# Kernel tuning notes

Measured on AMD Instinct MI355X. Metric: run time of the kernel, lower is better.

## Reference

```python
import jax, jax.numpy as jnp
import numpy as np

G, IN_DIM, OUT_DIM = 100000, 256, 128
B, N = 4096, 8192
ALPHA = 0.2          # LeakyReLU negative slope
NEG_INF = -9e15      # same masking constant as the torch module
EPS = 1e-12          # F.normalize eps


def setup_inputs() -> dict:
    key = jax.random.key(0)
    k1, k2, k3, k4, k5, k6, k7 = jax.random.split(key, 7)
    global_feature = jax.random.normal(k1, (G, IN_DIM), dtype=jnp.float32)
    nodes = jax.random.randint(k2, (B,), 0, G, dtype=jnp.int32)
    unique_nodes = jax.random.randint(k3, (N,), 0, G, dtype=jnp.int32)
    mask = jax.random.randint(k4, (B, N), 0, 2, dtype=jnp.int32)
    # ensure every row has at least one neighbor (original always includes self)
    mask = mask.at[:, 0].set(1)
    # xavier_uniform with gain=1.414
    gain = 1.414
    lim_W = gain * np.sqrt(6.0 / (IN_DIM + OUT_DIM))
    W = jax.random.uniform(k5, (IN_DIM, OUT_DIM), jnp.float32, -lim_W, lim_W)
    lim_a = gain * np.sqrt(6.0 / (2 * OUT_DIM + 1))
    a1 = jax.random.uniform(k6, (OUT_DIM,), jnp.float32, -lim_a, lim_a)
    a2 = jax.random.uniform(k7, (OUT_DIM,), jnp.float32, -lim_a, lim_a)
    return {"global_feature": global_feature, "nodes": nodes,
            "unique_nodes": unique_nodes, "mask": mask,
            "W": W, "a1": a1, "a2": a2}


def reference(global_feature, nodes, unique_nodes, mask, W, a1, a2):
    # project gathered features: [B,F], [N,F]
    h_nodes = global_feature[nodes] @ W
    h_neigh = global_feature[unique_nodes] @ W
    # additive attention scores; equivalent to cat([h_i,h_j]) @ a
    e = h_nodes @ a1[:, None] + (h_neigh @ a2)[None, :]   # [B,N]
    e = jnp.where(e >= 0, e, ALPHA * e)                    # leaky relu
    e = jnp.where(mask > 0, e, NEG_INF)
    attention = jax.nn.softmax(e, axis=1)                  # [B,N]
    out = attention @ h_neigh                              # [B,F]
    norm = jnp.linalg.norm(out, axis=1, keepdims=True)
    out = out / jnp.maximum(norm, EPS)                     # F.normalize p=2
    return out
```

## Files before the change

### kernel.cpp

```cpp
#include <hip/hip_runtime.h>
#include <hip/hip_bf16.h>

#define IN_DIM  256
#define OUT_DIM 128
#define B_ROWS  4096
#define N_COLS  8192
#define ALPHA   0.2f
#define NS      16

typedef unsigned short u16;
typedef unsigned int   u32;
typedef __attribute__((ext_vector_type(8))) short short8;
typedef __attribute__((ext_vector_type(4))) float floatx4;

__device__ __forceinline__ float bf2f(u16 v){ return __uint_as_float(((u32)v) << 16); }
__device__ __forceinline__ float bflo(u32 v){ return __uint_as_float(v << 16); }
__device__ __forceinline__ float bfhi(u32 v){ return __uint_as_float(v & 0xffff0000u); }
__device__ __forceinline__ u16 f2bf(float f){
    u32 u = __float_as_uint(f);
    u += 0x7fffu + ((u >> 16) & 1u);
    return (u16)(u >> 16);
}
__device__ __forceinline__ u32 pack_bf16(float a, float b){
    __hip_bfloat162 h = __float22bfloat162_rn(make_float2(a, b));
    return *reinterpret_cast<u32*>(&h);
}

__device__ __forceinline__ int detect_bf16_wave(const u32* __restrict__ g){
    int lane = threadIdx.x & 63;
    uint4 u = ((const uint4*)g)[lane];
#define CHK(x) ((((x) >> 7) & 0xFF) >= 110 && (((x) >> 7) & 0xFF) <= 140)
    unsigned long long c0 = __ballot(CHK(u.x)), c1 = __ballot(CHK(u.y));
    unsigned long long c2 = __ballot(CHK(u.z)), c3 = __ballot(CHK(u.w));
#undef CHK
    int votes = __popcll(c0) + __popcll(c1) + __popcll(c2) + __popcll(c3);
    return votes >= 128;
}

__global__ __launch_bounds__(128) void k_prep(const void* __restrict__ gf,
                                              const void* __restrict__ W, const void* __restrict__ a1,
                                              const void* __restrict__ a2,
                                              u16* __restrict__ WB, float* __restrict__ Wa1,
                                              float* __restrict__ a2f){
    const int isbf = detect_bf16_wave((const u32*)gf);
    const int c  = threadIdx.x;
    const int kb = blockIdx.x;
    float a1c = isbf ? bf2f(((const u16*)a1)[c]) : ((const float*)a1)[c];
    float w[8]; short8 v;
#pragma unroll
    for (int j = 0; j < 8; j++){
        w[j] = isbf ? bf2f(((const u16*)W)[(kb*8 + j) * OUT_DIM + c])
                    : ((const float*)W)[(kb*8 + j) * OUT_DIM + c];
        v[j] = (short)f2bf(w[j]);
    }
    ((short8*)WB)[kb * OUT_DIM + c] = v;

    __shared__ float red[2][8];
    int lane = c & 63, wv = c >> 6;
#pragma unroll
    for (int j = 0; j < 8; j++){
        float p = w[j] * a1c;
        p += __shfl_xor(p, 1);  p += __shfl_xor(p, 2);  p += __shfl_xor(p, 4);
        p += __shfl_xor(p, 8);  p += __shfl_xor(p, 16); p += __shfl_xor(p, 32);
        if (lane == 0) red[wv][j] = p;
    }
    __syncthreads();
    if (c < 8) Wa1[kb*8 + c] = red[0][c] + red[1][c];
    if (kb == 0) a2f[c] = isbf ? bf2f(((const u16*)a2)[c]) : ((const float*)a2)[c];
}

#define HN_BLKS 512
#define ESN_BLKS 1024
#define ZERO_BLKS 128
__global__ __launch_bounds__(256) void k_mid(const void* __restrict__ gf, const int* __restrict__ uniq,
                                             const int* __restrict__ nodes,
                                             const u16* __restrict__ WB, const float* __restrict__ a2f,
                                             const float* __restrict__ Wa1,
                                             u16* __restrict__ hB, float2* __restrict__ esg2,
                                             float2* __restrict__ esn2, float* __restrict__ oacc){
    const int bid = blockIdx.x;
    const int t   = threadIdx.x;

    if (bid < HN_BLKS){
        const int n0   = bid * 16;
        const int lane = t & 63;
        const int wv   = t >> 6;
        const int q    = lane >> 4;
        const int m    = lane & 15;
        const int isbf = detect_bf16_wave((const u32*)gf);
        const int jb0  = wv * 2;

        const size_t row = (size_t)uniq[n0 + m];
        const short8* wb8 = (const short8*)WB;

        floatx4 acc0 = {0.f,0.f,0.f,0.f};
        floatx4 acc1 = {0.f,0.f,0.f,0.f};

#pragma unroll
        for (int ks = 0; ks < IN_DIM/32; ks++){
            short8 afrag;
            if (isbf){
                afrag = *(const short8*)((const u16*)gf + row * IN_DIM + ks*32 + q*8);
            } else {
                const float* gp = (const float*)gf + row * IN_DIM + ks*32 + q*8;
                float4 f0 = *(const float4*)gp;
                float4 f1 = *(const float4*)(gp + 4);
                afrag[0] = (short)f2bf(f0.x); afrag[1] = (short)f2bf(f0.y);
                afrag[2] = (short)f2bf(f0.z); afrag[3] = (short)f2bf(f0.w);
                afrag[4] = (short)f2bf(f1.x); afrag[5] = (short)f2bf(f1.y);
                afrag[6] = (short)f2bf(f1.z); afrag[7] = (short)f2bf(f1.w);
            }
            const int kb = ks*4 + q;
            short8 b0 = wb8[kb * OUT_DIM + jb0*16 + m];
            short8 b1 = wb8[kb * OUT_DIM + (jb0+1)*16 + m];
            acc0 = __builtin_amdgcn_mfma_f32_16x16x32_bf16(afrag, b0, acc0, 0, 0, 0);
            acc1 = __builtin_amdgcn_mfma_f32_16x16x32_bf16(afrag, b1, acc1, 0, 0, 0);
        }

        {
            uint2 v0, v1;
            v0.x = pack_bf16(acc0[0], acc0[1]);
            v0.y = pack_bf16(acc0[2], acc0[3]);
            v1.x = pack_bf16(acc1[0], acc1[1]);
            v1.y = pack_bf16(acc1[2], acc1[3]);
            u16* base = hB + (size_t)(n0/8 + (q>>1)) * 1024 + (q&1)*4;
            *(uint2*)(base + (jb0*16 + m) * 8)     = v0;
            *(uint2*)(base + ((jb0+1)*16 + m) * 8) = v1;
        }

        __shared__ float sred[4][16];
        float a2c0 = a2f[jb0*16 + m], a2c1 = a2f[(jb0+1)*16 + m];
#pragma unroll
        for (int reg = 0; reg < 4; reg++){
            float pr = acc0[reg]*a2c0 + acc1[reg]*a2c1;
            pr += __shfl_xor(pr, 1); pr += __shfl_xor(pr, 2);
            pr += __shfl_xor(pr, 4); pr += __shfl_xor(pr, 8);
            if (m == 0) sred[wv][q*4 + reg] = pr;
        }
        __syncthreads();
        if (t < 16){
            float s = sred[0][t] + sred[1][t] + sred[2][t] + sred[3][t];
            s = fminf(fmaxf(s, -40.f), 40.f);
            esg2[n0 + t] = make_float2(__expf(s), __expf(ALPHA * s));
        }
    } else if (bid < HN_BLKS + ESN_BLKS){
        const int eb = bid - HN_BLKS;
        int lane = t & 63, wv = t >> 6;
        int b = eb * 4 + wv;
        const int isbf = detect_bf16_wave((const u32*)gf);
        float4 wa = ((const float4*)Wa1)[lane];
        float x0, x1, x2, x3;
        if (isbf){
            uint2 gg = ((const uint2*)((const u16*)gf + (size_t)nodes[b] * IN_DIM))[lane];
            x0 = bflo(gg.x); x1 = bfhi(gg.x); x2 = bflo(gg.y); x3 = bfhi(gg.y);
        } else {
            float4 gg = ((const float4*)((const float*)gf + (size_t)nodes[b] * IN_DIM))[lane];
            x0 = gg.x; x1 = gg.y; x2 = gg.z; x3 = gg.w;
        }
        float s = x0*wa.x + x1*wa.y + x2*wa.z + x3*wa.w;
        s += __shfl_xor(s, 1);  s += __shfl_xor(s, 2);  s += __shfl_xor(s, 4);
        s += __shfl_xor(s, 8);  s += __shfl_xor(s, 16); s += __shfl_xor(s, 32);
        if (lane == 0){
            s = fminf(fmaxf(s, -40.f), 40.f);
            esn2[b] = make_float2(__expf(s), __expf(ALPHA * s));
        }
    } else {
        const int zb = bid - (HN_BLKS + ESN_BLKS);
        float4* dst = (float4*)(oacc + (size_t)zb * (B_ROWS*OUT_DIM/ZERO_BLKS));
        float4 z = {0.f,0.f,0.f,0.f};
#pragma unroll
        for (int i = 0; i < 4; i++)
            dst[t + i*256] = z;
    }
}

template<int USE_PART>
__global__ __launch_bounds__(128, 4) void k_attn(const int* __restrict__ mask,
                                                 const float2* __restrict__ esn2,
                                                 const float2* __restrict__ esg2,
                                                 const u16* __restrict__ hB,
                                                 float* __restrict__ obuf){
    const int bid = blockIdx.x;
    const int ns  = bid & (NS-1);
    const int rg  = bid >> 4;
    const int t = threadIdx.x, lane = t & 63, wv = t >> 6;
    const int q = lane >> 4, m = lane & 15;
    const int rowbase = rg*32 + wv*16;
    const int row = rowbase + m;
    const int n0  = ns * (N_COLS/NS);

    __shared__ float4 seg[256];
    {
        const float4* egsrc = (const float4*)esg2 + (n0 >> 1);
        seg[t]       = egsrc[t];
        seg[t + 128] = egsrc[t + 128];
    }
    __syncthreads();

    const float2 en = esn2[row];
    const float enx = en.x, eny = en.y;
    const int* mrow = mask + (size_t)row * N_COLS;
    const short8* hb8 = (const short8*)hB;

    floatx4 acc[8];
#pragma unroll
    for (int jb = 0; jb < 8; jb++){ floatx4 z = {0.f,0.f,0.f,0.f}; acc[jb] = z; }

#pragma unroll 4
    for (int ks = 0; ks < 16; ks++){
        const int nn = n0 + ks*32;
        int4 ma = *(const int4*)(mrow + nn + q*8);
        int4 mb = *(const int4*)(mrow + nn + q*8 + 4);
        const float4* egl = &seg[ks*16 + q*4];
        float4 g0 = egl[0], g1 = egl[1], g2 = egl[2], g3 = egl[3];

        float p[8];
#define PEL(j, mk, gx, gy) { float tt = fmaxf(enx * (gx), eny * (gy)); \
                             p[j] = (mk) ? tt : 0.f; }
        PEL(0, ma.x, g0.x, g0.y) PEL(1, ma.y, g0.z, g0.w)
        PEL(2, ma.z, g1.x, g1.y) PEL(3, ma.w, g1.z, g1.w)
        PEL(4, mb.x, g2.x, g2.y) PEL(5, mb.y, g2.z, g2.w)
        PEL(6, mb.z, g3.x, g3.y) PEL(7, mb.w, g3.z, g3.w)
#undef PEL
        uint4 av;
        av.x = pack_bf16(p[0], p[1]); av.y = pack_bf16(p[2], p[3]);
        av.z = pack_bf16(p[4], p[5]); av.w = pack_bf16(p[6], p[7]);
        short8 af = *reinterpret_cast<short8*>(&av);

        const int kb = (nn >> 3) + q;
#pragma unroll
        for (int jb = 0; jb < 8; jb++){
            short8 bfr = hb8[kb * OUT_DIM + jb*16 + m];
            acc[jb] = __builtin_amdgcn_mfma_f32_16x16x32_bf16(af, bfr, acc[jb], 0, 0, 0);
        }
    }

    if (USE_PART){
        float* prow = obuf + (size_t)ns * (B_ROWS*OUT_DIM);
#pragma unroll
        for (int jb = 0; jb < 8; jb++)
#pragma unroll
            for (int reg = 0; reg < 4; reg++)
                prow[(size_t)(rowbase + q*4 + reg) * OUT_DIM + jb*16 + m] = acc[jb][reg];
    } else {
#pragma unroll
        for (int jb = 0; jb < 8; jb++)
#pragma unroll
            for (int reg = 0; reg < 4; reg++)
                atomicAdd(&obuf[(size_t)(rowbase + q*4 + reg) * OUT_DIM + jb*16 + m], acc[jb][reg]);
    }
}

template<int USE_PART>
__global__ __launch_bounds__(128) void k_norm(const float* __restrict__ obuf,
                                              const void* __restrict__ gf, void* __restrict__ out){
    const int isbf = detect_bf16_wave((const u32*)gf);
    const int b = blockIdx.x, c = threadIdx.x;
    float v;
    if (USE_PART){
        v = 0.f;
#pragma unroll
        for (int ns = 0; ns < NS; ns++)
            v += obuf[(size_t)ns * (B_ROWS*OUT_DIM) + (size_t)b * OUT_DIM + c];
    } else {
        v = obuf[(size_t)b * OUT_DIM + c];
    }
    float ss = v * v;
    for (int off = 32; off > 0; off >>= 1) ss += __shfl_down(ss, off);
    __shared__ float red[2];
    int lane = c & 63, wv = c >> 6;
    if (lane == 0) red[wv] = ss;
    __syncthreads();
    float tot = red[0] + red[1];
    float scale = 1.f / fmaxf(sqrtf(tot), 1e-12f);
    float o = v * scale;
    if (isbf) ((u16*)out)[(size_t)b * OUT_DIM + c] = f2bf(o);
    else      ((float*)out)[(size_t)b * OUT_DIM + c] = o;
}

extern "C" void kernel_launch(void* const* d_in, const int* in_sizes, int n_in,
                              void* d_out, int out_size, void* d_ws, size_t ws_size,
                              hipStream_t stream){
    const void* gf    = d_in[0];
    const int*  nodes = (const int*)d_in[1];
    const int*  uniq  = (const int*)d_in[2];
    const int*  mask  = (const int*)d_in[3];
    const void* W     = d_in[4];
    const void* a1    = d_in[5];
    const void* a2    = d_in[6];

    char* ws = (char*)d_ws;
    u16*    hB   = (u16*)ws;
    u16*    WB   = (u16*)(ws + (2u<<20));
    float2* esg2 = (float2*)(ws + (2u<<20) + (64u<<10));
    float*  Wa1  = (float*)(ws + (2u<<20) + (128u<<10));
    float*  a2f  = (float*)(ws + (2u<<20) + (129u<<10));
    float2* esn2 = (float2*)(ws + (2u<<20) + (130u<<10));
    float*  oacc = (float*)(ws + (4u<<20));
    float*  pbuf = (float*)(ws + (4u<<20));

    const int use_part = (ws_size >= (40u << 20)) ? 1 : 0;
    const int zero_blks = use_part ? 0 : ZERO_BLKS;

    hipLaunchKernelGGL(k_prep, dim3(32), dim3(128), 0, stream, gf, W, a1, a2, WB, Wa1, a2f);
    hipLaunchKernelGGL(k_mid,  dim3(HN_BLKS + ESN_BLKS + zero_blks), dim3(256), 0, stream,
                       gf, uniq, nodes, WB, a2f, Wa1, hB, esg2, esn2, oacc);
    if (use_part){
        hipLaunchKernelGGL(k_attn<1>, dim3((B_ROWS/32)*NS), dim3(128), 0, stream,
                           mask, esn2, esg2, hB, pbuf);
        hipLaunchKernelGGL(k_norm<1>, dim3(B_ROWS), dim3(128), 0, stream, pbuf, gf, d_out);
    } else {
        hipLaunchKernelGGL(k_attn<0>, dim3((B_ROWS/32)*NS), dim3(128), 0, stream,
                           mask, esn2, esg2, hB, oacc);
        hipLaunchKernelGGL(k_norm<0>, dim3(B_ROWS), dim3(128), 0, stream, oacc, gf, d_out);
    }
}
```

Before: 288.1 us.

## Pack int32 mask to bytes in prep pass and prefetch mask in attention loop

```diff
diff --git a/kernel.cpp b/kernel.cpp
--- a/kernel.cpp
+++ b/kernel.cpp
@@ -10,6 +10,7 @@
 
 typedef unsigned short u16;
 typedef unsigned int   u32;
+typedef unsigned char  u8;
 typedef __attribute__((ext_vector_type(8))) short short8;
 typedef __attribute__((ext_vector_type(4))) float floatx4;
 
@@ -69,6 +70,7 @@
     if (kb == 0) a2f[c] = isbf ? bf2f(((const u16*)a2)[c]) : ((const float*)a2)[c];
 }
 
+#define PK_BLKS 512
 #define HN_BLKS 512
 #define ESN_BLKS 1024
 #define ZERO_BLKS 128
@@ -77,9 +79,25 @@
                                              const u16* __restrict__ WB, const float* __restrict__ a2f,
                                              const float* __restrict__ Wa1,
                                              u16* __restrict__ hB, float2* __restrict__ esg2,
-                                             float2* __restrict__ esn2, float* __restrict__ oacc){
-    const int bid = blockIdx.x;
-    const int t   = threadIdx.x;
+                                             float2* __restrict__ esn2, float* __restrict__ oacc,
+                                             const int* __restrict__ mask, u8* __restrict__ bmask,
+                                             int pk_blks){
+    const int bid0 = blockIdx.x;
+    const int t    = threadIdx.x;
+
+    if (bid0 < pk_blks){
+        const uint4* src = (const uint4*)mask;
+        uchar4* dst = (uchar4*)bmask;
+        const size_t base = (size_t)bid0 * 256 + t;
+#pragma unroll 4
+        for (int it = 0; it < 64; it++){
+            size_t idx = base + (size_t)it * (PK_BLKS*256);
+            uint4 v = src[idx];
+            dst[idx] = make_uchar4(v.x ? 1 : 0, v.y ? 1 : 0, v.z ? 1 : 0, v.w ? 1 : 0);
+        }
+        return;
+    }
+    const int bid = bid0 - pk_blks;
 
     if (bid < HN_BLKS){
         const int n0   = bid * 16;
@@ -174,8 +192,9 @@
     }
 }
 
-template<int USE_PART>
+template<int MODE>
 __global__ __launch_bounds__(128, 4) void k_attn(const int* __restrict__ mask,
+                                                 const u8* __restrict__ bmask,
                                                  const float2* __restrict__ esn2,
                                                  const float2* __restrict__ esg2,
                                                  const u16* __restrict__ hB,
@@ -200,28 +219,55 @@
     const float2 en = esn2[row];
     const float enx = en.x, eny = en.y;
     const int* mrow = mask + (size_t)row * N_COLS;
+    const u8* brow  = bmask + (size_t)row * N_COLS + n0 + q*8;
     const short8* hb8 = (const short8*)hB;
 
     floatx4 acc[8];
 #pragma unroll
     for (int jb = 0; jb < 8; jb++){ floatx4 z = {0.f,0.f,0.f,0.f}; acc[jb] = z; }
+
+    uint2 bw; int4 ma, mb;
+    if (MODE == 2){
+        bw = *(const uint2*)(brow);
+    } else {
+        ma = *(const int4*)(mrow + n0 + q*8);
+        mb = *(const int4*)(mrow + n0 + q*8 + 4);
+    }
 
 #pragma unroll 4
     for (int ks = 0; ks < 16; ks++){
         const int nn = n0 + ks*32;
-        int4 ma = *(const int4*)(mrow + nn + q*8);
-        int4 mb = *(const int4*)(mrow + nn + q*8 + 4);
+        uint2 bwn = bw; int4 na = ma, nb = mb;
+        if (ks < 15){
+            if (MODE == 2){
+                bwn = *(const uint2*)(brow + (ks+1)*32);
+            } else {
+                na = *(const int4*)(mrow + nn + 32 + q*8);
+                nb = *(const int4*)(mrow + nn + 32 + q*8 + 4);
+            }
+        }
         const float4* egl = &seg[ks*16 + q*4];
         float4 g0 = egl[0], g1 = egl[1], g2 = egl[2], g3 = egl[3];
 
         float p[8];
+        if (MODE == 2){
+            const u32 wx = bw.x, wy = bw.y;
+#define PELB(j, w, sh, gx, gy) { float tt = fmaxf(enx * (gx), eny * (gy)); \
+                                 p[j] = (((w) >> (sh)) & 0xffu) ? tt : 0.f; }
+            PELB(0, wx, 0,  g0.x, g0.y) PELB(1, wx, 8,  g0.z, g0.w)
+            PELB(2, wx, 16, g1.x, g1.y) PELB(3, wx, 24, g1.z, g1.w)
+            PELB(4, wy, 0,  g2.x, g2.y) PELB(5, wy, 8,  g2.z, g2.w)
+            PELB(6, wy, 16, g3.x, g3.y) PELB(7, wy, 24, g3.z, g3.w)
+#undef PELB
+        } else {
 #define PEL(j, mk, gx, gy) { float tt = fmaxf(enx * (gx), eny * (gy)); \
                              p[j] = (mk) ? tt : 0.f; }
-        PEL(0, ma.x, g0.x, g0.y) PEL(1, ma.y, g0.z, g0.w)
-        PEL(2, ma.z, g1.x, g1.y) PEL(3, ma.w, g1.z, g1.w)
-        PEL(4, mb.x, g2.x, g2.y) PEL(5, mb.y, g2.z, g2.w)
-        PEL(6, mb.z, g3.x, g3.y) PEL(7, mb.w, g3.z, g3.w)
+            PEL(0, ma.x, g0.x, g0.y) PEL(1, ma.y, g0.z, g0.w)
+            PEL(2, ma.z, g1.x, g1.y) PEL(3, ma.w, g1.z, g1.w)
+            PEL(4, mb.x, g2.x, g2.y) PEL(5, mb.y, g2.z, g2.w)
+            PEL(6, mb.z, g3.x, g3.y) PEL(7, mb.w, g3.z, g3.w)
 #undef PEL
+        }
         uint4 av;
         av.x = pack_bf16(p[0], p[1]); av.y = pack_bf16(p[2], p[3]);
         av.z = pack_bf16(p[4], p[5]); av.w = pack_bf16(p[6], p[7]);
@@ -233,9 +279,10 @@
             short8 bfr = hb8[kb * OUT_DIM + jb*16 + m];
             acc[jb] = __builtin_amdgcn_mfma_f32_16x16x32_bf16(af, bfr, acc[jb], 0, 0, 0);
         }
-    }
-
-    if (USE_PART){
+        bw = bwn; ma = na; mb = nb;
+    }
+
+    if (MODE >= 1){
         float* prow = obuf + (size_t)ns * (B_ROWS*OUT_DIM);
 #pragma unroll
         for (int jb = 0; jb < 8; jb++)
@@ -298,20 +345,27 @@
     float2* esn2 = (float2*)(ws + (2u<<20) + (130u<<10));
     float*  oacc = (float*)(ws + (4u<<20));
     float*  pbuf = (float*)(ws + (4u<<20));
+    u8*     bmask= (u8*)(ws + (36u<<20));
 
     const int use_part = (ws_size >= (40u << 20)) ? 1 : 0;
+    const int use_bm   = (ws_size >= (72u << 20)) ? 1 : 0;
     const int zero_blks = use_part ? 0 : ZERO_BLKS;
+    const int pk = use_bm ? PK_BLKS : 0;
 
     hipLaunchKernelGGL(k_prep, dim3(32), dim3(128), 0, stream, gf, W, a1, a2, WB, Wa1, a2f);
-    hipLaunchKernelGGL(k_mid,  dim3(HN_BLKS + ESN_BLKS + zero_blks), dim3(256), 0, stream,
-                       gf, uniq, nodes, WB, a2f, Wa1, hB, esg2, esn2, oacc);
-    if (use_part){
+    hipLaunchKernelGGL(k_mid,  dim3(pk + HN_BLKS + ESN_BLKS + zero_blks), dim3(256), 0, stream,
+                       gf, uniq, nodes, WB, a2f, Wa1, hB, esg2, esn2, oacc, mask, bmask, pk);
+    if (use_bm){
+        hipLaunchKernelGGL(k_attn<2>, dim3((B_ROWS/32)*NS), dim3(128), 0, stream,
+                           mask, bmask, esn2, esg2, hB, pbuf);
+        hipLaunchKernelGGL(k_norm<1>, dim3(B_ROWS), dim3(128), 0, stream, pbuf, gf, d_out);
+    } else if (use_part){
         hipLaunchKernelGGL(k_attn<1>, dim3((B_ROWS/32)*NS), dim3(128), 0, stream,
-                           mask, esn2, esg2, hB, pbuf);
+                           mask, bmask, esn2, esg2, hB, pbuf);
         hipLaunchKernelGGL(k_norm<1>, dim3(B_ROWS), dim3(128), 0, stream, pbuf, gf, d_out);
     } else {
         hipLaunchKernelGGL(k_attn<0>, dim3((B_ROWS/32)*NS), dim3(128), 0, stream,
-                           mask, esn2, esg2, hB, oacc);
+                           mask, bmask, esn2, esg2, hB, oacc);
         hipLaunchKernelGGL(k_norm<0>, dim3(B_ROWS), dim3(128), 0, stream, oacc, gf, d_out);
     }
 }
```

Measured after the change: 292.4 us. No clear change (+1.5%).
